# Kernel tuning notes

Hardware: AMD Instinct MI355X
Metric: run time of the kernel (lower is better)

## Reference

```python
import jax, jax.numpy as jnp
import numpy as np

H2 = 128  # 2*hidden_dim

def setup_inputs() -> dict:
    key = jax.random.key(0)
    k1, k2, k3 = jax.random.split(key, 3)
    B, Lb, Lp = 64, 1024, 1024
    body = jax.random.normal(k1, (B, Lb, H2), dtype=jnp.float32)
    pun = jax.random.normal(k2, (B, Lp, H2), dtype=jnp.float32)
    w_u = jax.random.normal(k3, (3 * H2, 1), dtype=jnp.float32)
    return {"batch_size": B, "body": body, "pun": pun, "w_u": w_u}

def reference(batch_size, body, pun, w_u):
    # score[b,i,j] = [body_i ; pun_j ; body_i*pun_j] @ w_u
    # Decompose w_u into the three 128-dim blocks so the double loop fuses
    # into two matvecs plus one weighted batched GEMM.
    w = w_u[:, 0]
    w1, w2, w3 = w[:H2], w[H2:2 * H2], w[2 * H2:]
    s_body = jnp.einsum('bid,d->bi', body, w1)          # [B, Lb]
    s_pun = jnp.einsum('bjd,d->bj', pun, w2)            # [B, Lp]
    s_cross = jnp.einsum('bid,bjd->bij', body * w3, pun)  # [B, Lb, Lp]
    return s_cross + s_body[:, :, None] + s_pun[:, None, :]
```

## Files before the change

### kernel.cpp

```cpp
#include <hip/hip_runtime.h>


#define LSEQ 1024
#define H2K  128


typedef __attribute__((ext_vector_type(8))) short bfrag;
typedef __attribute__((ext_vector_type(4))) float f32x4;

__device__ __forceinline__ short f2bf(float x) {
    unsigned u = __float_as_uint(x);
    unsigned r = (u + 0x7fff + ((u >> 16) & 1)) >> 16;
    return (short)r;
}
__device__ __forceinline__ float bf2f(short s) {
    return __uint_as_float(((unsigned)(unsigned short)s) << 16);
}

__device__ __forceinline__ void ld16(void* lds, const void* g) {
    __builtin_amdgcn_global_load_lds(
        (const __attribute__((address_space(1))) void*)g,
        (__attribute__((address_space(3))) void*)lds, 16, 0, 0);
}

__global__ __launch_bounds__(256) void prep_kernel(
    const float* __restrict__ body, const float* __restrict__ pun,
    const float* __restrict__ w_u, float* __restrict__ ws)
{
    const int flag = blockIdx.y;
    const int lane = threadIdx.x & 63;
    const int wv   = threadIdx.x >> 6;
    const size_t row = (size_t)blockIdx.x * 4 + wv;

    const float* src = (flag ? pun : body) + row * H2K;
    const float2 v  = *(const float2*)(src + lane * 2);
    const float2 wm = *(const float2*)(w_u + flag * H2K + lane * 2);

    float p = v.x * wm.x + v.y * wm.y;
    p += __shfl_xor(p, 32);
    p += __shfl_xor(p, 16);
    p += __shfl_xor(p, 8);
    p += __shfl_xor(p, 4);
    p += __shfl_xor(p, 2);
    p += __shfl_xor(p, 1);
    if (lane == 0) ws[(size_t)flag * 65536 + row] = p;

    float cx = v.x, cy = v.y;
    if (!flag) {
        const float2 w3v = *(const float2*)(w_u + 2 * H2K + lane * 2);
        cx *= w3v.x; cy *= w3v.y;
    }
    const short h0 = f2bf(cx), h1 = f2bf(cy);
    const short l0 = f2bf(cx - bf2f(h0)), l1 = f2bf(cy - bf2f(h1));

    short* hb = (short*)(ws + 131072) + (size_t)flag * 16777216 + row * H2K + lane * 2;
    *(unsigned*)hb =
        ((unsigned)(unsigned short)h0) | ((unsigned)(unsigned short)h1 << 16);
    *(unsigned*)(hb + 8388608) =
        ((unsigned)(unsigned short)l0) | ((unsigned)(unsigned short)l1 << 16);
}

__global__ __launch_bounds__(512, 4) void align_mfma(
    const float* __restrict__ ws, float* __restrict__ out)
{
    __shared__ __align__(16) short Ch[2][4096], Cl[2][4096];
    __shared__ __align__(16) short Ph[2][4096], Pl[2][4096];

    const int bb = blockIdx.z;
    const int ti = blockIdx.y * 128;
    const int tj = blockIdx.x * 128;
    const int t    = threadIdx.x;
    const int lane = t & 63;
    const int w    = t >> 6;

    const int srow = w * 16 + (lane & 15);
    const int k8   = lane >> 4;
    const short* base = (const short*)(ws + 131072);
    const size_t crow = (size_t)(bb * LSEQ + ti + srow) * H2K + k8 * 8;
    const size_t prow = (size_t)(bb * LSEQ + tj + srow) * H2K + k8 * 8;
    const short* gCh = base + crow;
    const short* gCl = base + 8388608 + crow;
    const short* gPh = base + 16777216 + prow;
    const short* gPl = base + 25165824 + prow;

    const int mt0 = (w >> 1) * 2;
    const int nt0 = (w & 1) * 4;
    f32x4 acc[2][4] = {};

    ld16(&Ch[0][t * 8], gCh);
    ld16(&Cl[0][t * 8], gCl);
    ld16(&Ph[0][t * 8], gPh);
    ld16(&Pl[0][t * 8], gPl);

#pragma unroll
    for (int kt = 0; kt < 4; ++kt) {
        const int cur = kt & 1, nxt = cur ^ 1;

        if (kt < 3) {
            ld16(&Ch[nxt][t * 8], gCh + (kt + 1) * 32);
            ld16(&Cl[nxt][t * 8], gCl + (kt + 1) * 32);
            ld16(&Ph[nxt][t * 8], gPh + (kt + 1) * 32);
            ld16(&Pl[nxt][t * 8], gPl + (kt + 1) * 32);
        }
        __builtin_amdgcn_sched_barrier(0);
        if (kt < 3) asm volatile("s_waitcnt vmcnt(4)" ::: "memory");
        else        asm volatile("s_waitcnt vmcnt(0)" ::: "memory");
        __builtin_amdgcn_s_barrier();

        bfrag ph[2], pl[2], ch[4], cl[4];
#pragma unroll
        for (int i = 0; i < 2; ++i) {
            ph[i] = *(const bfrag*)&Ph[cur][((mt0 + i) * 64 + lane) * 8];
            pl[i] = *(const bfrag*)&Pl[cur][((mt0 + i) * 64 + lane) * 8];
        }
#pragma unroll
        for (int j = 0; j < 4; ++j) {
            ch[j] = *(const bfrag*)&Ch[cur][((nt0 + j) * 64 + lane) * 8];
            cl[j] = *(const bfrag*)&Cl[cur][((nt0 + j) * 64 + lane) * 8];
        }
#pragma unroll
        for (int i = 0; i < 2; ++i)
#pragma unroll
            for (int j = 0; j < 4; ++j) {
                acc[i][j] = __builtin_amdgcn_mfma_f32_16x16x32_bf16(ph[i], ch[j], acc[i][j], 0, 0, 0);
                acc[i][j] = __builtin_amdgcn_mfma_f32_16x16x32_bf16(ph[i], cl[j], acc[i][j], 0, 0, 0);
                acc[i][j] = __builtin_amdgcn_mfma_f32_16x16x32_bf16(pl[i], ch[j], acc[i][j], 0, 0, 0);
            }

        if (kt < 3) __builtin_amdgcn_s_barrier();
        __builtin_amdgcn_sched_barrier(0);
    }

    const float* sbp = ws + (size_t)bb * LSEQ;
    const float* spp = ws + 65536 + (size_t)bb * LSEQ;
    const int q = lane >> 4, ln = lane & 15;
#pragma unroll
    for (int mi = 0; mi < 2; ++mi) {
        const int j0 = tj + (mt0 + mi) * 16 + q * 4;
        const float4 spv = *(const float4*)(spp + j0);
#pragma unroll
        for (int ni = 0; ni < 4; ++ni) {
            const int row = ti + (nt0 + ni) * 16 + ln;
            const float sb = sbp[row];
            const f32x4 a = acc[mi][ni];
            float4 r = { a[0] + sb + spv.x, a[1] + sb + spv.y,
                         a[2] + sb + spv.z, a[3] + sb + spv.w };
            *(float4*)&out[((size_t)bb * LSEQ + row) * LSEQ + j0] = r;
        }
    }
}

extern "C" void kernel_launch(void* const* d_in, const int* in_sizes, int n_in,
                              void* d_out, int out_size, void* d_ws, size_t ws_size,
                              hipStream_t stream) {
    const float* body = (const float*)d_in[1];
    const float* pun  = (const float*)d_in[2];
    const float* w_u  = (const float*)d_in[3];
    float* out = (float*)d_out;
    float* ws  = (float*)d_ws;
    const int B = in_sizes[1] / (LSEQ * H2K);

    dim3 g1((B * LSEQ) / 4, 2, 1);
    prep_kernel<<<g1, 256, 0, stream>>>(body, pun, w_u, ws);

    dim3 g2(LSEQ / 128, LSEQ / 128, B);
    align_mfma<<<g2, 512, 0, stream>>>(ws, out);
}
```

Before: 402.2 us.

## Enlarge MFMA output tile to 256x256 and remap blocks with XCD-aware swizzle

The GEMM tile grows from 128x128 to 256x256 per workgroup, so each wave now holds 32 accumulators instead of 8 and reuses its P fragments across more C fragments. LDS per block doubles and occupancy drops to 2 blocks per CU. The grid is flattened to 1D with a bid&7 remap that groups tiles per XCD for better L2 locality. The aim is to cut global/LDS traffic per FLOP, at the cost of higher register pressure and fewer resident waves to hide store and load latency.

```diff
diff --git a/kernel.cpp b/kernel.cpp
--- a/kernel.cpp
+++ b/kernel.cpp
@@ -60,15 +60,19 @@
         ((unsigned)(unsigned short)l0) | ((unsigned)(unsigned short)l1 << 16);
 }
 
-__global__ __launch_bounds__(512, 4) void align_mfma(
+__global__ __launch_bounds__(512, 2) void align_mfma(
     const float* __restrict__ ws, float* __restrict__ out)
 {
-    __shared__ __align__(16) short Ch[2][4096], Cl[2][4096];
-    __shared__ __align__(16) short Ph[2][4096], Pl[2][4096];
+    __shared__ __align__(16) short Ch[2][8192], Cl[2][8192];
+    __shared__ __align__(16) short Ph[2][8192], Pl[2][8192];
 
-    const int bb = blockIdx.z;
-    const int ti = blockIdx.y * 128;
-    const int tj = blockIdx.x * 128;
+    const int nwg = gridDim.x;
+    const int bid = blockIdx.x;
+    const int tid = (bid & 7) * (nwg >> 3) + (bid >> 3);
+    const int bb = tid >> 4;
+    const int ti = ((tid >> 2) & 3) * 256;
+    const int tj = (tid & 3) * 256;
+
     const int t    = threadIdx.x;
     const int lane = t & 63;
     const int w    = t >> 6;
@@ -82,67 +86,70 @@
     const short* gCl = base + 8388608 + crow;
     const short* gPh = base + 16777216 + prow;
     const short* gPl = base + 25165824 + prow;
+    const size_t R2 = (size_t)128 * H2K;
 
-    const int mt0 = (w >> 1) * 2;
-    const int nt0 = (w & 1) * 4;
-    f32x4 acc[2][4] = {};
+#define STAGE(u, c) do {                                         \
+        ld16(&Ch[u][t * 8],         gCh + (c) * 32);             \
+        ld16(&Ch[u][(512 + t) * 8], gCh + R2 + (c) * 32);        \
+        ld16(&Cl[u][t * 8],         gCl + (c) * 32);             \
+        ld16(&Cl[u][(512 + t) * 8], gCl + R2 + (c) * 32);        \
+        ld16(&Ph[u][t * 8],         gPh + (c) * 32);             \
+        ld16(&Ph[u][(512 + t) * 8], gPh + R2 + (c) * 32);        \
+        ld16(&Pl[u][t * 8],         gPl + (c) * 32);             \
+        ld16(&Pl[u][(512 + t) * 8], gPl + R2 + (c) * 32);        \
+    } while (0)
 
-    ld16(&Ch[0][t * 8], gCh);
-    ld16(&Cl[0][t * 8], gCl);
-    ld16(&Ph[0][t * 8], gPh);
-    ld16(&Pl[0][t * 8], gPl);
+    const int jg = w & 1;
+    const int ig = w >> 1;
+    f32x4 acc[8][4] = {};
+
+    STAGE(0, 0);
 
 #pragma unroll
     for (int kt = 0; kt < 4; ++kt) {
         const int cur = kt & 1, nxt = cur ^ 1;
 
-        if (kt < 3) {
-            ld16(&Ch[nxt][t * 8], gCh + (kt + 1) * 32);
-            ld16(&Cl[nxt][t * 8], gCl + (kt + 1) * 32);
-            ld16(&Ph[nxt][t * 8], gPh + (kt + 1) * 32);
-            ld16(&Pl[nxt][t * 8], gPl + (kt + 1) * 32);
-        }
+        if (kt < 3) STAGE(nxt, kt + 1);
         __builtin_amdgcn_sched_barrier(0);
-        if (kt < 3) asm volatile("s_waitcnt vmcnt(4)" ::: "memory");
+        if (kt < 3) asm volatile("s_waitcnt vmcnt(8)" ::: "memory");
         else        asm volatile("s_waitcnt vmcnt(0)" ::: "memory");
         __builtin_amdgcn_s_barrier();
 
-        bfrag ph[2], pl[2], ch[4], cl[4];
+        bfrag ph[8], pl[8];
 #pragma unroll
-        for (int i = 0; i < 2; ++i) {
-            ph[i] = *(const bfrag*)&Ph[cur][((mt0 + i) * 64 + lane) * 8];
-            pl[i] = *(const bfrag*)&Pl[cur][((mt0 + i) * 64 + lane) * 8];
+        for (int jj = 0; jj < 8; ++jj) {
+            ph[jj] = *(const bfrag*)&Ph[cur][((jg * 8 + jj) * 64 + lane) * 8];
+            pl[jj] = *(const bfrag*)&Pl[cur][((jg * 8 + jj) * 64 + lane) * 8];
         }
 #pragma unroll
-        for (int j = 0; j < 4; ++j) {
-            ch[j] = *(const bfrag*)&Ch[cur][((nt0 + j) * 64 + lane) * 8];
-            cl[j] = *(const bfrag*)&Cl[cur][((nt0 + j) * 64 + lane) * 8];
+        for (int ii = 0; ii < 4; ++ii) {
+            const bfrag ch = *(const bfrag*)&Ch[cur][((ig * 4 + ii) * 64 + lane) * 8];
+            const bfrag cl = *(const bfrag*)&Cl[cur][((ig * 4 + ii) * 64 + lane) * 8];
+#pragma unroll
+            for (int jj = 0; jj < 8; ++jj) {
+                acc[jj][ii] = __builtin_amdgcn_mfma_f32_16x16x32_bf16(ph[jj], ch, acc[jj][ii], 0, 0, 0);
+                acc[jj][ii] = __builtin_amdgcn_mfma_f32_16x16x32_bf16(ph[jj], cl, acc[jj][ii], 0, 0, 0);
+                acc[jj][ii] = __builtin_amdgcn_mfma_f32_16x16x32_bf16(pl[jj], ch, acc[jj][ii], 0, 0, 0);
+            }
         }
-#pragma unroll
-        for (int i = 0; i < 2; ++i)
-#pragma unroll
-            for (int j = 0; j < 4; ++j) {
-                acc[i][j] = __builtin_amdgcn_mfma_f32_16x16x32_bf16(ph[i], ch[j], acc[i][j], 0, 0, 0);
-                acc[i][j] = __builtin_amdgcn_mfma_f32_16x16x32_bf16(ph[i], cl[j], acc[i][j], 0, 0, 0);
-                acc[i][j] = __builtin_amdgcn_mfma_f32_16x16x32_bf16(pl[i], ch[j], acc[i][j], 0, 0, 0);
-            }
 
         if (kt < 3) __builtin_amdgcn_s_barrier();
         __builtin_amdgcn_sched_barrier(0);
     }
+#undef STAGE
 
     const float* sbp = ws + (size_t)bb * LSEQ;
     const float* spp = ws + 65536 + (size_t)bb * LSEQ;
-    const int q = lane >> 4, ln = lane & 15;
+    const int qd = lane >> 4, ln = lane & 15;
 #pragma unroll
-    for (int mi = 0; mi < 2; ++mi) {
-        const int j0 = tj + (mt0 + mi) * 16 + q * 4;
+    for (int jj = 0; jj < 8; ++jj) {
+        const int j0 = tj + (jg * 8 + jj) * 16 + qd * 4;
         const float4 spv = *(const float4*)(spp + j0);
 #pragma unroll
-        for (int ni = 0; ni < 4; ++ni) {
-            const int row = ti + (nt0 + ni) * 16 + ln;
+        for (int ii = 0; ii < 4; ++ii) {
+            const int row = ti + (ig * 4 + ii) * 16 + ln;
             const float sb = sbp[row];
-            const f32x4 a = acc[mi][ni];
+            const f32x4 a = acc[jj][ii];
             float4 r = { a[0] + sb + spv.x, a[1] + sb + spv.y,
                          a[2] + sb + spv.z, a[3] + sb + spv.w };
             *(float4*)&out[((size_t)bb * LSEQ + row) * LSEQ + j0] = r;
@@ -163,6 +170,6 @@
     dim3 g1((B * LSEQ) / 4, 2, 1);
     prep_kernel<<<g1, 256, 0, stream>>>(body, pun, w_u, ws);
 
-    dim3 g2(LSEQ / 128, LSEQ / 128, B);
+    dim3 g2(B * 16, 1, 1);
     align_mfma<<<g2, 512, 0, stream>>>(ws, out);
 }
```

Measured after the change: 410.6 us. 2.1% more time.
